# Performance work log

Hardware: AMD Instinct MI355X
Metric: run time of the kernel (lower is better)

The kernel has to match this reference:

```python
import jax, jax.numpy as jnp
import numpy as np

B, N, C, H = 8, 1025, 1024, 16
DH = C // H
HID = 4 * C
EPS = 1e-5
NEG = -65504.0


def _ln(x, g, b):
    mu = jnp.mean(x, axis=-1, keepdims=True)
    var = jnp.mean(jnp.square(x - mu), axis=-1, keepdims=True)
    return (x - mu) * jax.lax.rsqrt(var + EPS) * g + b


def setup_inputs() -> dict:
    key = jax.random.key(0)
    ks = jax.random.split(key, 12)
    s = 0.02
    return {
        "x": jax.random.normal(ks[0], (B, N, C), jnp.float32),
        "rel_pos_bias": jax.random.normal(ks[1], (H, N, N), jnp.float32),
        "attn_mask": jnp.zeros((B, N, N), jnp.bool_),
        "ln1_g": jnp.ones((C,), jnp.float32),
        "ln1_b": jnp.zeros((C,), jnp.float32),
        "qkv_w": jax.random.normal(ks[2], (C, 3 * C), jnp.float32) * s,
        "qkv_b": jnp.zeros((3 * C,), jnp.float32),
        "proj_w": jax.random.normal(ks[3], (C, C), jnp.float32) * s,
        "proj_b": jnp.zeros((C,), jnp.float32),
        "ln2_g": jnp.ones((C,), jnp.float32),
        "ln2_b": jnp.zeros((C,), jnp.float32),
        "fc1_w": jax.random.normal(ks[4], (C, HID), jnp.float32) * s,
        "fc1_b": jnp.zeros((HID,), jnp.float32),
        "fc2_w": jax.random.normal(ks[5], (HID, C), jnp.float32) * s,
        "fc2_b": jnp.zeros((C,), jnp.float32),
    }


def reference(x, rel_pos_bias, attn_mask, ln1_g, ln1_b, qkv_w, qkv_b,
              proj_w, proj_b, ln2_g, ln2_b, fc1_w, fc1_b, fc2_w, fc2_b):
    scale = DH ** -0.5
    # --- attention branch ---
    h = _ln(x, ln1_g, ln1_b)
    qkv = (h @ qkv_w + qkv_b).reshape(B, N, 3, H, DH)
    q, k, v = [jnp.transpose(qkv[:, :, i], (0, 2, 1, 3)) for i in range(3)]  # [B,H,N,DH]
    attn = jnp.einsum('bhnd,bhmd->bhnm', q * scale, k)
    attn = jnp.where(attn_mask[:, None], NEG, attn)
    attn = attn + rel_pos_bias  # [H,N,N] broadcasts over batch
    attn_wo_softmax = attn
    a = jax.nn.softmax(attn, axis=-1)
    o = jnp.einsum('bhnm,bhmd->bhnd', a, v)
    o = jnp.transpose(o, (0, 2, 1, 3)).reshape(B, N, C)
    o = o @ proj_w + proj_b
    x = x + o
    # --- MLP branch ---
    h2 = _ln(x, ln2_g, ln2_b)
    h2 = jax.nn.gelu(h2 @ fc1_w + fc1_b, approximate=False)
    x = x + (h2 @ fc2_w + fc2_b)
    return (x, attn_wo_softmax)
```

## Files before the change

kernel.cpp:

```cpp
#include <hip/hip_runtime.h>
#include <math.h>

typedef unsigned short u16;
typedef unsigned char u8;
typedef unsigned int u32;
typedef __attribute__((ext_vector_type(4))) float f32x4;
typedef __attribute__((ext_vector_type(4), aligned(4))) float f32x4u;
typedef __attribute__((ext_vector_type(8))) short s16x8;

#define DEV __device__ __forceinline__

constexpr int BB = 8, NN = 1025, CC = 1024, HH = 16;
constexpr int NP  = 1152;
constexpr int MP  = 8320;
constexpr int TOK = BB * NN;
constexpr int MW  = 36;
constexpr float NEGV = -65504.f;

DEV u16 f2bf(float f){ union { float f; unsigned u; } v; v.f = f; return (u16)((v.u + 0x7fffu + ((v.u >> 16) & 1u)) >> 16); }
DEV float bf2f(u16 u){ union { float f; unsigned u; } v; v.u = (unsigned)u << 16; return v.f; }
DEV u32 cvt_pk_bf16(float lo_, float hi_){
  u32 r; asm("v_cvt_pk_bf16_f32 %0, %1, %2" : "=v"(r) : "v"(lo_), "v"(hi_)); return r;
}

struct __align__(8) us4 { u16 x, y, z, w; };

typedef const __attribute__((address_space(1))) void gv_t;
typedef __attribute__((address_space(3))) void lv_t;
DEV void gload16(const void* g, void* l){
  __builtin_amdgcn_global_load_lds((gv_t*)g, (lv_t*)l, 16, 0, 0);
}

__launch_bounds__(256)
__global__ void cvt_transpose(const float* __restrict__ W, u16* __restrict__ Wt, int K, int Nn){
  __shared__ float tile[32][33];
  const int n0 = blockIdx.x * 32, k0 = blockIdx.y * 32;
  const int tx = threadIdx.x & 31, ty = threadIdx.x >> 5;
#pragma unroll
  for (int i = 0; i < 4; i++)
    tile[ty + i * 8][tx] = W[(size_t)(k0 + ty + i * 8) * Nn + n0 + tx];
  __syncthreads();
#pragma unroll
  for (int i = 0; i < 4; i++){
    const int n = n0 + ty + i * 8;
    Wt[(size_t)n * K + k0 + tx] = f2bf(tile[tx][ty + i * 8]);
  }
}

__launch_bounds__(256)
__global__ void ln_kernel(const float* __restrict__ x, const float* __restrict__ g,
                          const float* __restrict__ b, u16* __restrict__ out, int validRows){
  const int row = blockIdx.x, tid = threadIdx.x;
  const size_t base = (size_t)row * CC + tid * 4;
  if (row >= validRows){ us4 z{0,0,0,0}; *(us4*)(out + base) = z; return; }
  f32x4u v = *(const f32x4u*)(x + base);
  float s  = v[0] + v[1] + v[2] + v[3];
  float ss = v[0]*v[0] + v[1]*v[1] + v[2]*v[2] + v[3]*v[3];
#pragma unroll
  for (int o = 32; o; o >>= 1){ s += __shfl_xor(s, o, 64); ss += __shfl_xor(ss, o, 64); }
  __shared__ float ps[4], pq[4];
  if ((tid & 63) == 0){ ps[tid >> 6] = s; pq[tid >> 6] = ss; }
  __syncthreads();
  s  = ps[0] + ps[1] + ps[2] + ps[3];
  ss = pq[0] + pq[1] + pq[2] + pq[3];
  const float mu = s * (1.f / CC);
  const float rs = rsqrtf(ss * (1.f / CC) - mu * mu + 1e-5f);
  f32x4u gv = *(const f32x4u*)(g + tid * 4);
  f32x4u bv = *(const f32x4u*)(b + tid * 4);
  us4 o;
  o.x = f2bf((v[0]-mu)*rs*gv[0] + bv[0]);
  o.y = f2bf((v[1]-mu)*rs*gv[1] + bv[1]);
  o.z = f2bf((v[2]-mu)*rs*gv[2] + bv[2]);
  o.w = f2bf((v[3]-mu)*rs*gv[3] + bv[3]);
  *(us4*)(out + base) = o;
}

template<int MODE>
__launch_bounds__(256)
__global__ void gemm_nt(const u16* __restrict__ A, const u16* __restrict__ Bt,
                        const float* __restrict__ bias, int K, int Nw,
                        const float* __restrict__ resid, float* __restrict__ fout,
                        u16* __restrict__ bout){
  __shared__ u16 As[128 * 32];
  __shared__ u16 Bs[128 * 32];
  const int tid = threadIdx.x;
  const int w = tid >> 6, l = tid & 63;
  const int wr = w >> 1, wc = w & 1;
  const int row0 = blockIdx.y * 128, col0 = blockIdx.x * 128;
  f32x4 acc[4][4] = {};
  for (int k0 = 0; k0 < K; k0 += 32){
    __syncthreads();
#pragma unroll
    for (int j = 0; j < 2; j++){
      const int ch = tid + j * 256;
      const int r = ch >> 2, co = (ch & 3) * 8;
      gload16(A  + (size_t)(row0 + r) * K + k0 + co, As + (size_t)ch * 8);
      gload16(Bt + (size_t)(col0 + r) * K + k0 + co, Bs + (size_t)ch * 8);
    }
    __syncthreads();
    s16x8 af[4], bf[4];
#pragma unroll
    for (int m = 0; m < 4; m++)
      af[m] = *(const s16x8*)(As + (wr * 64 + m * 16 + (l & 15)) * 32 + (l >> 4) * 8);
#pragma unroll
    for (int n = 0; n < 4; n++)
      bf[n] = *(const s16x8*)(Bs + (wc * 64 + n * 16 + (l & 15)) * 32 + (l >> 4) * 8);
#pragma unroll
    for (int m = 0; m < 4; m++)
#pragma unroll
      for (int n = 0; n < 4; n++)
        acc[m][n] = __builtin_amdgcn_mfma_f32_16x16x32_bf16(af[m], bf[n], acc[m][n], 0, 0, 0);
  }
#pragma unroll
  for (int m = 0; m < 4; m++){
#pragma unroll
    for (int n = 0; n < 4; n++){
      const int c = col0 + wc * 64 + n * 16 + (l & 15);
      const float bs = bias[c];
#pragma unroll
      for (int j = 0; j < 4; j++){
        const int r = row0 + wr * 64 + m * 16 + ((l >> 4) << 2) + j;
        float v = acc[m][n][j] + bs;
        if (MODE == 0){
          bout[(size_t)r * Nw + c] = f2bf(v);
        } else if (MODE == 1){
          const float xi = (r < TOK) ? resid[(size_t)r * CC + c] : 0.f;
          fout[(size_t)r * CC + c] = xi + v;
        } else if (MODE == 2){
          const float gx = 0.5f * v * (1.f + erff(v * 0.70710678118654752f));
          bout[(size_t)r * Nw + c] = f2bf(gx);
        } else {
          if (r < TOK) fout[(size_t)r * CC + c] = resid[(size_t)r * CC + c] + v;
        }
      }
    }
  }
}

__launch_bounds__(256)
__global__ void reorder_qkv(const u16* __restrict__ qkv, u16* __restrict__ q,
                            u16* __restrict__ k, u16* __restrict__ vT){
  __shared__ u16 vt[64][65];
  const int bh = blockIdx.y, b = bh >> 4, h = bh & 15;
  const int n0 = blockIdx.x * 64;
  const int tid = threadIdx.x;
  const int d = tid & 63, nl = tid >> 6;
#pragma unroll
  for (int i = 0; i < 16; i++){
    const int nlocal = nl * 16 + i;
    const int n = n0 + nlocal;
    u16 qv = 0, kv = 0, vv = 0;
    if (n < NN){
      const size_t t = (size_t)b * NN + n;
      const u16* p = qkv + t * 3072 + h * 64 + d;
      qv = f2bf(bf2f(p[0]) * 0.125f);
      kv = p[1024];
      vv = p[2048];
    }
    q[(size_t)bh * NP * 64 + (size_t)n * 64 + d] = qv;
    k[(size_t)bh * NP * 64 + (size_t)n * 64 + d] = kv;
    vt[nlocal][d] = vv;
  }
  __syncthreads();
#pragma unroll
  for (int i = 0; i < 16; i++){
    const int dd = (tid >> 6) * 16 + i;
    const int nn2 = tid & 63;
    vT[(size_t)bh * 64 * NP + (size_t)dd * NP + n0 + nn2] = vt[nn2][dd];
  }
}

__launch_bounds__(256)
__global__ void mask_pack(const u8* __restrict__ mask, u32* __restrict__ mbits){
  const int idx = blockIdx.x * 256 + threadIdx.x;
  if (idx >= BB * NP * MW) return;
  const int word = idx % MW;
  const int row  = (idx / MW) % NP;
  const int b    = idx / (MW * NP);
  u32 bits = 0;
  if (row < NN){
    const u8* mrow = mask + (size_t)b * NN * NN + (size_t)row * NN;
    const int c0 = word * 32;
    const int lim = (NN - c0 < 32) ? (NN - c0) : 32;
    for (int j = 0; j < lim; j++) bits |= (u32)(mrow[c0 + j] != 0) << j;
  }
  mbits[idx] = bits;
}

__launch_bounds__(512)
__global__ void attn_flash(const u16* __restrict__ q, const u16* __restrict__ k,
                           const u16* __restrict__ vT, const float* __restrict__ bias,
                           const u32* __restrict__ mbits,
                           float* __restrict__ S, u16* __restrict__ obuf){
  __shared__ u16 Ks[2][128 * 64];
  __shared__ u16 Vs[2][64 * 128];

  const int f = blockIdx.x;
  const int xcd = f & 7, ii = f >> 3;
  const int hl = ii / 72, rem = ii % 72;
  const int rt = rem >> 3, b = rem & 7;
  const int h = xcd * 2 + hl;
  const int bh = b * 16 + h;
  const int tid = threadIdx.x, w = tid >> 6, l = tid & 63;
  const int lg = l >> 4, lo = l & 15;
  const int row0 = rt * 128 + w * 16;
  const u16* qb = q + (size_t)bh * NP * 64;
  const u16* kb = k + (size_t)bh * NP * 64;
  const u16* vb = vT + (size_t)bh * 64 * NP;
  const float* bias_h = bias + (size_t)h * NN * NN;
  const u32* mrow_b = mbits + (size_t)b * NP * MW;
  float* Sb = S + (size_t)bh * NN * NN;

  s16x8 qf[2];
#pragma unroll
  for (int kk = 0; kk < 2; kk++)
    qf[kk] = *(const s16x8*)(qb + (size_t)(row0 + lo) * 64 + kk * 32 + lg * 8);

  float m_run = -1e30f, l_run = 0.f;
  f32x4 acc_o[4] = {};

  auto stage = [&](int buf, int ct){
    const int cb = ct * 128;
#pragma unroll
    for (int i = 0; i < 2; i++){
      const int chunk = tid + i * 512;
      const int row = chunk >> 3, cs = chunk & 7;
      const int cg = cs ^ (row & 7);
      gload16(kb + (size_t)(cb + row) * 64 + cg * 8, Ks[buf] + (size_t)chunk * 8);
    }
#pragma unroll
    for (int i = 0; i < 2; i++){
      const int chunk = tid + i * 512;
      const int row = chunk >> 4, cs = chunk & 15;
      const int cg = cs ^ (row & 15);
      gload16(vb + (size_t)row * NP + cb + cg * 8, Vs[buf] + (size_t)chunk * 8);
    }
  };

  stage(0, 0);

  for (int ct = 0; ct < 9; ct++){
    const int cb = ct * 128;
    const int cur = ct & 1;
    if (ct < 8){
      stage(cur ^ 1, ct + 1);
      asm volatile("s_waitcnt vmcnt(4)" ::: "memory");
    } else {
      asm volatile("s_waitcnt vmcnt(0)" ::: "memory");
    }
    __builtin_amdgcn_s_barrier();
    __builtin_amdgcn_sched_barrier(0);
    const u16* KsC = Ks[cur];
    const u16* VsC = Vs[cur];

    f32x4 sa[8] = {};
    __builtin_amdgcn_s_setprio(1);
#pragma unroll
    for (int m2 = 0; m2 < 8; m2++){
      const int rl = (m2 >> 1) * 32 + (lo >> 2) * 8 + (m2 & 1) * 4 + (lo & 3);
      const s16x8 kf0 = *(const s16x8*)(KsC + rl * 64 + ((lg ^ (rl & 7)) << 3));
      const s16x8 kf1 = *(const s16x8*)(KsC + rl * 64 + (((4 + lg) ^ (rl & 7)) << 3));
      sa[m2] = __builtin_amdgcn_mfma_f32_16x16x32_bf16(kf0, qf[0], sa[m2], 0, 0, 0);
      sa[m2] = __builtin_amdgcn_mfma_f32_16x16x32_bf16(kf1, qf[1], sa[m2], 0, 0, 0);
    }
    __builtin_amdgcn_s_setprio(0);
    {
      const int qr = row0 + lo;
      if (qr < NN){
        const u32* mrp = mrow_b + (size_t)qr * MW + ct * 4;
        u32 mb[4];
#pragma unroll
        for (int i = 0; i < 4; i++) mb[i] = mrp[i];
        const float* brow = bias_h + (size_t)qr * NN;
        float* srow = Sb + (size_t)qr * NN;
#pragma unroll
        for (int m2 = 0; m2 < 8; m2++){
          const int kc0 = cb + (m2 >> 1) * 32 + lg * 8 + (m2 & 1) * 4;
          const u32 bits = mb[m2 >> 1] >> (lg * 8 + (m2 & 1) * 4);
          f32x4 a = sa[m2];
          if (kc0 + 3 < NN){
            f32x4u bv = *(const f32x4u*)(brow + kc0);
#pragma unroll
            for (int jj = 0; jj < 4; jj++){
              float v = ((bits >> jj) & 1u) ? NEGV : a[jj];
              a[jj] = v + bv[jj];
            }
            *(f32x4u*)(srow + kc0) = a;
          } else {
#pragma unroll
            for (int jj = 0; jj < 4; jj++){
              if (kc0 + jj < NN){
                float v = ((bits >> jj) & 1u) ? NEGV : a[jj];
                v += brow[kc0 + jj];
                srow[kc0 + jj] = v;
                a[jj] = v;
              } else a[jj] = -1e30f;
            }
          }
          sa[m2] = a;
        }
      } else {
        const f32x4 z = {0.f, 0.f, 0.f, 0.f};
#pragma unroll
        for (int m2 = 0; m2 < 8; m2++) sa[m2] = z;
      }
    }
    float sc;
    {
      float mt = -1e30f;
#pragma unroll
      for (int m2 = 0; m2 < 8; m2++){
        f32x4 a = sa[m2];
        mt = fmaxf(mt, fmaxf(fmaxf(a[0], a[1]), fmaxf(a[2], a[3])));
      }
      mt = fmaxf(mt, __shfl_xor(mt, 16, 64));
      mt = fmaxf(mt, __shfl_xor(mt, 32, 64));
      const float mn = fmaxf(m_run, mt);
      sc = __expf(m_run - mn);
      float p = 0.f;
#pragma unroll
      for (int m2 = 0; m2 < 8; m2++){
        f32x4 a = sa[m2];
        const float e0 = __expf(a[0] - mn), e1 = __expf(a[1] - mn);
        const float e2 = __expf(a[2] - mn), e3 = __expf(a[3] - mn);
        p += (e0 + e1) + (e2 + e3);
        sa[m2][0] = __uint_as_float(cvt_pk_bf16(e0, e1));
        sa[m2][1] = __uint_as_float(cvt_pk_bf16(e2, e3));
      }
      p += __shfl_xor(p, 16, 64);
      p += __shfl_xor(p, 32, 64);
      l_run = l_run * sc + p;
      m_run = mn;
    }
#pragma unroll
    for (int jj = 0; jj < 4; jj++){
      const float s = __shfl(sc, (l & 48) + lg * 4 + jj, 64);
#pragma unroll
      for (int nd = 0; nd < 4; nd++) acc_o[nd][jj] *= s;
    }
    __builtin_amdgcn_s_setprio(1);
#pragma unroll
    for (int kc = 0; kc < 4; kc++){
      union { u32 d[4]; s16x8 v8; } af;
      af.d[0] = __float_as_uint(sa[2 * kc][0]);
      af.d[1] = __float_as_uint(sa[2 * kc][1]);
      af.d[2] = __float_as_uint(sa[2 * kc + 1][0]);
      af.d[3] = __float_as_uint(sa[2 * kc + 1][1]);
#pragma unroll
      for (int nd = 0; nd < 4; nd++){
        const int vrow = nd * 16 + lo;
        const s16x8 vf = *(const s16x8*)(VsC + vrow * 128 + (((kc * 4 + lg) ^ (vrow & 15)) << 3));
        acc_o[nd] = __builtin_amdgcn_mfma_f32_16x16x32_bf16(af.v8, vf, acc_o[nd], 0, 0, 0);
      }
    }
    __builtin_amdgcn_s_setprio(0);
    __builtin_amdgcn_s_barrier();
    __builtin_amdgcn_sched_barrier(0);
  }
  {
    const float li = 1.f / l_run;
#pragma unroll
    for (int jj = 0; jj < 4; jj++){
      const float il = __shfl(li, (l & 48) + lg * 4 + jj, 64);
      const int qr = row0 + lg * 4 + jj;
      if (qr < NN){
        const size_t base = ((size_t)b * NN + qr) * CC + (size_t)h * 64;
#pragma unroll
        for (int nd = 0; nd < 4; nd++)
          obuf[base + nd * 16 + lo] = f2bf(acc_o[nd][jj] * il);
      }
    }
  }
}

__launch_bounds__(256)
__global__ void zero_pad_rows(u16* __restrict__ buf){
  const size_t i = (size_t)blockIdx.x * 256 + threadIdx.x;
  buf[(size_t)TOK * CC + i] = 0;
}

extern "C" void kernel_launch(void* const* d_in, const int* in_sizes, int n_in,
                              void* d_out, int out_size, void* d_ws, size_t ws_size,
                              hipStream_t stream){
  const float* x     = (const float*)d_in[0];
  const float* rpb   = (const float*)d_in[1];
  const u8*    mask  = (const u8*)d_in[2];
  const float* ln1g  = (const float*)d_in[3];
  const float* ln1b  = (const float*)d_in[4];
  const float* qkvw  = (const float*)d_in[5];
  const float* qkvb  = (const float*)d_in[6];
  const float* projw = (const float*)d_in[7];
  const float* projb = (const float*)d_in[8];
  const float* ln2g  = (const float*)d_in[9];
  const float* ln2b  = (const float*)d_in[10];
  const float* fc1w  = (const float*)d_in[11];
  const float* fc1b  = (const float*)d_in[12];
  const float* fc2w  = (const float*)d_in[13];
  const float* fc2b  = (const float*)d_in[14];

  float* out_x = (float*)d_out;
  float* out_S = out_x + (size_t)BB * NN * CC;

  char* wsb = (char*)d_ws;
  size_t off = 0;
  auto alloc = [&](size_t bytes) -> char* {
    char* p = wsb + off; off += (bytes + 255) & ~(size_t)255; return p;
  };
  u16* h1     = (u16*)alloc((size_t)MP * CC * 2);
  u16* qkvbuf = (u16*)alloc((size_t)MP * 3072 * 2);
  u16* h3     = h1;
  u16* qkvwt  = (u16*)alloc((size_t)3072 * 1024 * 2);
  u16* projwt = (u16*)alloc((size_t)1024 * 1024 * 2);
  u16* fc1wt  = (u16*)alloc((size_t)4096 * 1024 * 2);
  u16* fc2wt  = (u16*)alloc((size_t)1024 * 4096 * 2);
  u16* qq     = (u16*)alloc((size_t)128 * NP * 64 * 2);
  u16* kk     = (u16*)alloc((size_t)128 * NP * 64 * 2);
  u16* vT     = (u16*)alloc((size_t)128 * 64 * NP * 2);
  u32* mbits  = (u32*)alloc((size_t)BB * NP * MW * 4);
  u16* obuf   = (u16*)alloc((size_t)MP * CC * 2);
  float* x1   = (float*)alloc((size_t)MP * CC * 4);
  u16* h2in   = (u16*)alloc((size_t)MP * CC * 2);

  cvt_transpose<<<dim3(3072/32, 1024/32), 256, 0, stream>>>(qkvw, qkvwt, 1024, 3072);
  cvt_transpose<<<dim3(1024/32, 1024/32), 256, 0, stream>>>(projw, projwt, 1024, 1024);
  cvt_transpose<<<dim3(4096/32, 1024/32), 256, 0, stream>>>(fc1w, fc1wt, 1024, 4096);
  cvt_transpose<<<dim3(1024/32, 4096/32), 256, 0, stream>>>(fc2w, fc2wt, 4096, 1024);
  ln_kernel<<<MP, 256, 0, stream>>>(x, ln1g, ln1b, h1, TOK);
  gemm_nt<0><<<dim3(3072/128, MP/128), 256, 0, stream>>>(h1, qkvwt, qkvb, 1024, 3072, nullptr, nullptr, qkvbuf);
  reorder_qkv<<<dim3(NP/64, 128), 256, 0, stream>>>(qkvbuf, qq, kk, vT);
  mask_pack<<<(BB * NP * MW + 255) / 256, 256, 0, stream>>>(mask, mbits);
  zero_pad_rows<<<(MP - TOK) * CC / 256, 256, 0, stream>>>(obuf);
  attn_flash<<<dim3(1152), 512, 0, stream>>>(qq, kk, vT, rpb, mbits, out_S, obuf);
  gemm_nt<1><<<dim3(1024/128, MP/128), 256, 0, stream>>>(obuf, projwt, projb, 1024, 1024, x, x1, nullptr);
  ln_kernel<<<MP, 256, 0, stream>>>(x1, ln2g, ln2b, h2in, TOK);
  gemm_nt<2><<<dim3(4096/128, MP/128), 256, 0, stream>>>(h2in, fc1wt, fc1b, 1024, 4096, nullptr, nullptr, h3);
  gemm_nt<3><<<dim3(1024/128, MP/128), 256, 0, stream>>>(h3, fc2wt, fc2b, 4096, 1024, x1, out_x, nullptr);
}
```

Before: 789.1 us.

## Double-buffer LDS tiles in bf16 GEMM to overlap global loads with MFMA

The GEMM kernel now keeps two LDS buffers for A and B tiles and issues the direct-to-LDS loads for the next K-step before computing on the current one. Explicit vmcnt waits and raw s_barrier calls replace the two __syncthreads per iteration. The aim is to hide global-memory latency behind the MFMA work in the QKV, proj and MLP GEMMs. It doubles LDS use per block, which may lower occupancy. It also depends on the hand-written vmcnt count matching the number of outstanding loads.

```diff
diff --git a/kernel.cpp b/kernel.cpp
--- a/kernel.cpp
+++ b/kernel.cpp
@@ -81,35 +81,52 @@
                         const float* __restrict__ bias, int K, int Nw,
                         const float* __restrict__ resid, float* __restrict__ fout,
                         u16* __restrict__ bout){
-  __shared__ u16 As[128 * 32];
-  __shared__ u16 Bs[128 * 32];
+  __shared__ u16 As[2][128 * 32];
+  __shared__ u16 Bs[2][128 * 32];
   const int tid = threadIdx.x;
   const int w = tid >> 6, l = tid & 63;
   const int wr = w >> 1, wc = w & 1;
   const int row0 = blockIdx.y * 128, col0 = blockIdx.x * 128;
-  f32x4 acc[4][4] = {};
-  for (int k0 = 0; k0 < K; k0 += 32){
-    __syncthreads();
+
+  auto stage = [&](int buf, int k0){
 #pragma unroll
     for (int j = 0; j < 2; j++){
       const int ch = tid + j * 256;
       const int r = ch >> 2, co = (ch & 3) * 8;
-      gload16(A  + (size_t)(row0 + r) * K + k0 + co, As + (size_t)ch * 8);
-      gload16(Bt + (size_t)(col0 + r) * K + k0 + co, Bs + (size_t)ch * 8);
-    }
-    __syncthreads();
+      gload16(A  + (size_t)(row0 + r) * K + k0 + co, As[buf] + (size_t)ch * 8);
+      gload16(Bt + (size_t)(col0 + r) * K + k0 + co, Bs[buf] + (size_t)ch * 8);
+    }
+  };
+
+  f32x4 acc[4][4] = {};
+  stage(0, 0);
+  int it = 0;
+  for (int k0 = 0; k0 < K; k0 += 32, ++it){
+    const int cur = it & 1;
+    if (k0 + 32 < K){
+      stage(cur ^ 1, k0 + 32);
+      asm volatile("s_waitcnt vmcnt(4)" ::: "memory");
+    } else {
+      asm volatile("s_waitcnt vmcnt(0)" ::: "memory");
+    }
+    __builtin_amdgcn_s_barrier();
+    __builtin_amdgcn_sched_barrier(0);
+    const u16* AsC = As[cur];
+    const u16* BsC = Bs[cur];
     s16x8 af[4], bf[4];
 #pragma unroll
     for (int m = 0; m < 4; m++)
-      af[m] = *(const s16x8*)(As + (wr * 64 + m * 16 + (l & 15)) * 32 + (l >> 4) * 8);
+      af[m] = *(const s16x8*)(AsC + (wr * 64 + m * 16 + (l & 15)) * 32 + (l >> 4) * 8);
 #pragma unroll
     for (int n = 0; n < 4; n++)
-      bf[n] = *(const s16x8*)(Bs + (wc * 64 + n * 16 + (l & 15)) * 32 + (l >> 4) * 8);
+      bf[n] = *(const s16x8*)(BsC + (wc * 64 + n * 16 + (l & 15)) * 32 + (l >> 4) * 8);
 #pragma unroll
     for (int m = 0; m < 4; m++)
 #pragma unroll
       for (int n = 0; n < 4; n++)
         acc[m][n] = __builtin_amdgcn_mfma_f32_16x16x32_bf16(af[m], bf[n], acc[m][n], 0, 0, 0);
+    __builtin_amdgcn_s_barrier();
+    __builtin_amdgcn_sched_barrier(0);
   }
 #pragma unroll
   for (int m = 0; m < 4; m++){
```

Result: faster. 765.1 us (-3.0%).
